# Kernel tuning notes

Measured on AMD Instinct MI355X. Metric: run time of the kernel, lower is better.

Reference implementation:

```python
import jax, jax.numpy as jnp
import numpy as np

D_MODEL = 1024
EXPAND = 2
D_INNER = D_MODEL * EXPAND
KERNEL = 4
EPS = 1e-5


def setup_inputs() -> dict:
    key = jax.random.key(0)
    ks = jax.random.split(key, 8)
    B, L = 2, 4096
    x = jax.random.normal(ks[0], (B, L, D_MODEL), dtype=jnp.float32)
    norm_w = jnp.ones((D_MODEL,), jnp.float32)
    norm_b = jnp.zeros((D_MODEL,), jnp.float32)
    # torch Linear weight layout [out, in]
    in_proj_w = jax.random.normal(ks[1], (2 * D_INNER, D_MODEL), jnp.float32) / np.sqrt(D_MODEL)
    # depthwise Conv1d weight [d_inner, 1, K]
    conv_w = jax.random.normal(ks[2], (D_INNER, 1, KERNEL), jnp.float32) / np.sqrt(KERNEL)
    conv_b = jax.random.normal(ks[3], (D_INNER,), jnp.float32) * 0.02
    gate_w = jax.random.normal(ks[4], (D_INNER, D_INNER), jnp.float32) / np.sqrt(D_INNER)
    gate_b = jnp.zeros((D_INNER,), jnp.float32)
    out_proj_w = jax.random.normal(ks[5], (D_MODEL, D_INNER), jnp.float32) / np.sqrt(D_INNER)
    return {"x": x, "norm_w": norm_w, "norm_b": norm_b, "in_proj_w": in_proj_w,
            "conv_w": conv_w, "conv_b": conv_b, "gate_w": gate_w, "gate_b": gate_b,
            "out_proj_w": out_proj_w}


def _layernorm(x, w, b):
    mu = jnp.mean(x, axis=-1, keepdims=True)
    var = jnp.var(x, axis=-1, keepdims=True)
    return (x - mu) * jax.lax.rsqrt(var + EPS) * w + b


def _glru(x, norm_w, norm_b, in_proj_w, conv_w, conv_b, gate_w, gate_b, out_proj_w):
    B, L, D = x.shape
    residual = x
    xn = _layernorm(x, norm_w, norm_b)
    xz = jnp.einsum('bld,ed->ble', xn, in_proj_w)  # [B,L,2*d_inner]
    x_inner, z = jnp.split(xz, 2, axis=-1)
    # causal depthwise conv: torch pads 3 both sides then slices [:L] == left-pad 3
    lhs = jnp.transpose(x_inner, (0, 2, 1))  # [B, C, L]
    conv = jax.lax.conv_general_dilated(
        lhs, conv_w, window_strides=(1,), padding=[(KERNEL - 1, 0)],
        feature_group_count=D_INNER,
        dimension_numbers=('NCH', 'OIH', 'NCH'))
    x_conv = jnp.transpose(conv, (0, 2, 1)) + conv_b  # [B, L, C]
    x_conv = jax.nn.silu(x_conv)
    a = jax.nn.sigmoid(jnp.einsum('blc,ec->ble', x_conv, gate_w) + gate_b)
    b = (1.0 - a) * x_conv
    # h_t = a_t * h_{t-1} + b_t, h_0 prior = 0 -> parallel associative scan
    def combine(e1, e2):
        a1, b1 = e1
        a2, b2 = e2
        return a1 * a2, a2 * b1 + b2
    _, y = jax.lax.associative_scan(combine, (a, b), axis=1)
    y = y * jax.nn.silu(z)
    return residual + jnp.einsum('blc,dc->bld', y, out_proj_w)


def reference(x, norm_w, norm_b, in_proj_w, conv_w, conv_b, gate_w, gate_b, out_proj_w):
    return _glru(x, norm_w, norm_b, in_proj_w, conv_w, conv_b, gate_w, gate_b, out_proj_w)
```

## Files before the change

### kernel.cpp

```cpp
#include <hip/hip_runtime.h>
#include <cstdint>

#define D_MODEL 1024
#define D_INNER 2048
#define LSEQ    4096
#define BATCH   2
#define M_ROWS  (BATCH * LSEQ)
#define CHUNK   128
#define NCHUNK  (LSEQ / CHUNK)

typedef unsigned short u16;
typedef __bf16 bf16x8 __attribute__((ext_vector_type(8)));
typedef float f32x4 __attribute__((ext_vector_type(4)));
typedef u16 u16x4 __attribute__((ext_vector_type(4)));

__device__ __forceinline__ u16 f2bf(float f) {
  union { float f; unsigned u; } x; x.f = f;
  unsigned u = x.u;
  unsigned r = (u + 0x7FFFu + ((u >> 16) & 1u)) >> 16;
  return (u16)r;
}
__device__ __forceinline__ float bf2f(u16 h) {
  union { unsigned u; float f; } x; x.u = ((unsigned)h) << 16;
  return x.f;
}
__device__ __forceinline__ float sigmoidf_(float v) { return 1.0f / (1.0f + expf(-v)); }
__device__ __forceinline__ float siluf_(float v)    { return v / (1.0f + expf(-v)); }

__device__ __forceinline__ void gl_lds16(const void* g, void* l) {
  __builtin_amdgcn_global_load_lds(
      (const __attribute__((address_space(1))) void*)g,
      (__attribute__((address_space(3))) void*)l, 16, 0, 0);
}

#define SBAR()   asm volatile("s_barrier" ::: "memory")
#define WAITV0() asm volatile("s_waitcnt vmcnt(0)" ::: "memory")
#define WAITL0() do { asm volatile("s_waitcnt lgkmcnt(0)" ::: "memory"); __builtin_amdgcn_sched_barrier(0); } while (0)

__global__ void __launch_bounds__(256)
cast_bf16_kernel(const float* __restrict__ in, u16* __restrict__ out, int n4) {
  int i = blockIdx.x * 256 + threadIdx.x;
  if (i < n4) {
    float4 v = ((const float4*)in)[i];
    u16x4 o;
    o.x = f2bf(v.x); o.y = f2bf(v.y); o.z = f2bf(v.z); o.w = f2bf(v.w);
    ((u16x4*)out)[i] = o;
  }
}

__global__ void __launch_bounds__(256)
ln_kernel(const float* __restrict__ x, const float* __restrict__ w,
          const float* __restrict__ b, u16* __restrict__ xn) {
  const int row = blockIdx.x;
  const int t = threadIdx.x;
  const float4 v = ((const float4*)(x + (size_t)row * D_MODEL))[t];
  float s  = v.x + v.y + v.z + v.w;
  float ss = v.x * v.x + v.y * v.y + v.z * v.z + v.w * v.w;
#pragma unroll
  for (int o = 32; o > 0; o >>= 1) {
    s  += __shfl_xor(s, o);
    ss += __shfl_xor(ss, o);
  }
  __shared__ float red[8];
  const int wid = t >> 6, lane = t & 63;
  if (lane == 0) { red[wid] = s; red[4 + wid] = ss; }
  __syncthreads();
  s  = red[0] + red[1] + red[2] + red[3];
  ss = red[4] + red[5] + red[6] + red[7];
  const float mu  = s * (1.0f / D_MODEL);
  const float var = ss * (1.0f / D_MODEL) - mu * mu;
  const float rs  = rsqrtf(var + 1e-5f);
  const float4 wv = ((const float4*)w)[t];
  const float4 bv = ((const float4*)b)[t];
  u16x4 o4;
  o4.x = f2bf((v.x - mu) * rs * wv.x + bv.x);
  o4.y = f2bf((v.y - mu) * rs * wv.y + bv.y);
  o4.z = f2bf((v.z - mu) * rs * wv.z + bv.z);
  o4.w = f2bf((v.w - mu) * rs * wv.w + bv.w);
  ((u16x4*)(xn + (size_t)row * D_MODEL))[t] = o4;
}

#define MFMA_BF16 __builtin_amdgcn_mfma_f32_16x16x32_bf16

template<int EPI>
__global__ void __launch_bounds__(512, 2)
gemm256(const u16* __restrict__ A, const u16* __restrict__ Bm,
        int M, int N, int K,
        const float* __restrict__ ef, float* __restrict__ of,
        u16* __restrict__ ob0, u16* __restrict__ ob1) {
  __shared__ __align__(1024) char lds[131072];
  const int tid  = threadIdx.x;
  const int wid  = tid >> 6, lane = tid & 63;
  const int nbx  = N >> 8;
  const int nwg  = nbx * (M >> 8);
  const int bid  = blockIdx.x;
  const int cpx  = nwg >> 3;
  const int swz  = (bid & 7) * cpx + (bid >> 3);
  const int bx   = swz % nbx, by = swz / nbx;
  const size_t m0 = (size_t)by << 8, n0 = (size_t)bx << 8;

  const int wr = wid >> 2, wc = wid & 3;
  const size_t rb = (size_t)K * 2;
  const size_t rj = (size_t)64 * rb;

  const int srow  = lane >> 3;
  const int sslot = ((lane & 7) ^ srow) << 4;
  const char* gA = (const char*)A  + (m0 + (size_t)(wid * 8 + srow)) * rb + sslot;
  const char* gB = (const char*)Bm + (n0 + (size_t)(wid * 8 + srow)) * rb + sslot;
  const int sdst = wid * 1024;

  const int q    = lane >> 4;
  const int r15  = lane & 15;
  const int cswz0 = (q * 16)      ^ ((lane & 7) << 4);
  const int cswz1 = (64 + q * 16) ^ ((lane & 7) << 4);
  const int paoff = (wr * 128 + r15) * 128;
  const int pboff = (wc * 64  + r15) * 128;

  f32x4 acc[8][4] = {};
  const int nk = K >> 6;

  {
    const char* a = gA; const char* b = gB;
#pragma unroll
    for (int i = 0; i < 4; ++i) {
      gl_lds16(a, lds + sdst + i * 8192);
      gl_lds16(b, lds + 65536 + sdst + i * 8192);
      a += rj; b += rj;
    }
  }
  WAITV0();
  SBAR();

  int kb = 128;
  for (int t = 0; t < nk; ++t) {
    const int cur = t & 1;
    const char* At = lds + cur * 32768;
    const char* Bt = lds + 65536 + cur * 32768;
    char* An = lds + (cur ^ 1) * 32768;
    char* Bn = lds + 65536 + (cur ^ 1) * 32768;
    const bool pf = (t + 1 < nk);

    bf16x8 af[4][2], b0[2][2], b1[2][2];

    if (pf) {
      gl_lds16(gA + kb,      An + sdst);
      gl_lds16(gA + kb + rj, An + sdst + 8192);
      gl_lds16(gB + kb,      Bn + sdst);
      gl_lds16(gB + kb + rj, Bn + sdst + 8192);
    }
#pragma unroll
    for (int mi = 0; mi < 4; ++mi) {
      af[mi][0] = *(const bf16x8*)(At + paoff + mi * 2048 + cswz0);
      af[mi][1] = *(const bf16x8*)(At + paoff + mi * 2048 + cswz1);
    }
#pragma unroll
    for (int ni = 0; ni < 2; ++ni) {
      b0[ni][0] = *(const bf16x8*)(Bt + pboff + ni * 2048 + cswz0);
      b0[ni][1] = *(const bf16x8*)(Bt + pboff + ni * 2048 + cswz1);
    }
    SBAR();
    WAITL0();
    __builtin_amdgcn_s_setprio(1);
#pragma unroll
    for (int mi = 0; mi < 4; ++mi)
#pragma unroll
      for (int ni = 0; ni < 2; ++ni) {
        acc[mi][ni] = MFMA_BF16(af[mi][0], b0[ni][0], acc[mi][ni], 0, 0, 0);
        acc[mi][ni] = MFMA_BF16(af[mi][1], b0[ni][1], acc[mi][ni], 0, 0, 0);
      }
    __builtin_amdgcn_s_setprio(0);
    SBAR();

    if (pf) {
      gl_lds16(gA + kb + 2 * rj, An + sdst + 16384);
      gl_lds16(gA + kb + 3 * rj, An + sdst + 24576);
      gl_lds16(gB + kb + 2 * rj, Bn + sdst + 16384);
      gl_lds16(gB + kb + 3 * rj, Bn + sdst + 24576);
    }
#pragma unroll
    for (int ni = 0; ni < 2; ++ni) {
      b1[ni][0] = *(const bf16x8*)(Bt + pboff + (ni + 2) * 2048 + cswz0);
      b1[ni][1] = *(const bf16x8*)(Bt + pboff + (ni + 2) * 2048 + cswz1);
    }
    SBAR();
    WAITL0();
    __builtin_amdgcn_s_setprio(1);
#pragma unroll
    for (int mi = 0; mi < 4; ++mi)
#pragma unroll
      for (int ni = 0; ni < 2; ++ni) {
        acc[mi][ni + 2] = MFMA_BF16(af[mi][0], b1[ni][0], acc[mi][ni + 2], 0, 0, 0);
        acc[mi][ni + 2] = MFMA_BF16(af[mi][1], b1[ni][1], acc[mi][ni + 2], 0, 0, 0);
      }
    __builtin_amdgcn_s_setprio(0);
    SBAR();

#pragma unroll
    for (int mi = 0; mi < 4; ++mi) {
      af[mi][0] = *(const bf16x8*)(At + paoff + (mi + 4) * 2048 + cswz0);
      af[mi][1] = *(const bf16x8*)(At + paoff + (mi + 4) * 2048 + cswz1);
    }
    SBAR();
    WAITL0();
    __builtin_amdgcn_s_setprio(1);
#pragma unroll
    for (int mi = 0; mi < 4; ++mi)
#pragma unroll
      for (int ni = 0; ni < 2; ++ni) {
        acc[mi + 4][ni] = MFMA_BF16(af[mi][0], b0[ni][0], acc[mi + 4][ni], 0, 0, 0);
        acc[mi + 4][ni] = MFMA_BF16(af[mi][1], b0[ni][1], acc[mi + 4][ni], 0, 0, 0);
      }
    __builtin_amdgcn_s_setprio(0);
    SBAR();

    __builtin_amdgcn_s_setprio(1);
#pragma unroll
    for (int mi = 0; mi < 4; ++mi)
#pragma unroll
      for (int ni = 0; ni < 2; ++ni) {
        acc[mi + 4][ni + 2] = MFMA_BF16(af[mi][0], b1[ni][0], acc[mi + 4][ni + 2], 0, 0, 0);
        acc[mi + 4][ni + 2] = MFMA_BF16(af[mi][1], b1[ni][1], acc[mi + 4][ni + 2], 0, 0, 0);
      }
    __builtin_amdgcn_s_setprio(0);
    if (pf) WAITV0();
    SBAR();
    kb += 128;
  }

  const int c0 = lane & 15;
  const int r0 = (lane >> 4) << 2;
#pragma unroll
  for (int mi = 0; mi < 8; ++mi) {
#pragma unroll
    for (int ni = 0; ni < 4; ++ni) {
#pragma unroll
      for (int rg = 0; rg < 4; ++rg) {
        const size_t row = m0 + (size_t)(wr * 128 + mi * 16 + r0 + rg);
        const size_t col = n0 + (size_t)(wc * 64 + ni * 16 + c0);
        const float v = acc[mi][ni][rg];
        if (EPI == 0) {
          if (col < (size_t)D_INNER) ob0[row * D_INNER + col] = f2bf(v);
          else                       ob1[row * D_INNER + (col - D_INNER)] = f2bf(siluf_(v));
        } else if (EPI == 1) {
          of[row * (size_t)N + col] = sigmoidf_(v + ef[col]);
        } else {
          of[row * (size_t)N + col] = v + ef[row * (size_t)N + col];
        }
      }
    }
  }
}

__global__ void __launch_bounds__(256)
conv_silu_kernel(const u16* __restrict__ xin, const float* __restrict__ cw,
                 const float* __restrict__ cb, u16* __restrict__ xc) {
  const int c   = blockIdx.x * 256 + threadIdx.x;
  const int l0  = blockIdx.y * 8;
  const int bat = blockIdx.z;
  const size_t base = ((size_t)bat * LSEQ) * D_INNER + c;
  const float w0 = cw[c * 4 + 0], w1 = cw[c * 4 + 1], w2 = cw[c * 4 + 2], w3 = cw[c * 4 + 3];
  const float bb = cb[c];
  float v[11];
#pragma unroll
  for (int i = 0; i < 11; ++i) {
    const int l = l0 - 3 + i;
    v[i] = (l >= 0) ? bf2f(xin[base + (size_t)l * D_INNER]) : 0.0f;
  }
#pragma unroll
  for (int r = 0; r < 8; ++r) {
    const float acc = bb + w0 * v[r] + w1 * v[r + 1] + w2 * v[r + 2] + w3 * v[r + 3];
    xc[base + (size_t)(l0 + r) * D_INNER] = f2bf(siluf_(acc));
  }
}

__global__ void __launch_bounds__(256)
scan_a_kernel(const float* __restrict__ a, const u16* __restrict__ xc,
              float* __restrict__ cA, float* __restrict__ cB) {
  const int c   = blockIdx.x * 256 + threadIdx.x;
  const int ch  = blockIdx.y;
  const int bat = blockIdx.z;
  size_t idx = ((size_t)bat * LSEQ + (size_t)ch * CHUNK) * D_INNER + c;
  float pA = 1.0f, hB = 0.0f;
  for (int t = 0; t < CHUNK; ++t) {
    const float av = a[idx];
    const float bv = (1.0f - av) * bf2f(xc[idx]);
    pA *= av;
    hB = av * hB + bv;
    idx += D_INNER;
  }
  const size_t o = ((size_t)bat * NCHUNK + ch) * D_INNER + c;
  cA[o] = pA; cB[o] = hB;
}

__global__ void __launch_bounds__(256)
scan_b_kernel(const float* __restrict__ cA, const float* __restrict__ cB,
              float* __restrict__ carry) {
  const int tid = blockIdx.x * 256 + threadIdx.x;
  const int bat = tid >> 11;
  const int c   = tid & (D_INNER - 1);
  float h = 0.0f;
  const size_t base = (size_t)bat * NCHUNK * D_INNER + c;
  for (int i = 0; i < NCHUNK; ++i) {
    const size_t o = base + (size_t)i * D_INNER;
    carry[o] = h;
    h = cA[o] * h + cB[o];
  }
}

__global__ void __launch_bounds__(256)
scan_c_kernel(const float* __restrict__ a, const u16* __restrict__ xc,
              const u16* __restrict__ sz, const float* __restrict__ carry,
              u16* __restrict__ yg) {
  const int c   = blockIdx.x * 256 + threadIdx.x;
  const int ch  = blockIdx.y;
  const int bat = blockIdx.z;
  float h = carry[((size_t)bat * NCHUNK + ch) * D_INNER + c];
  size_t idx = ((size_t)bat * LSEQ + (size_t)ch * CHUNK) * D_INNER + c;
  for (int t = 0; t < CHUNK; ++t) {
    const float av = a[idx];
    const float bv = (1.0f - av) * bf2f(xc[idx]);
    h = av * h + bv;
    yg[idx] = f2bf(h * bf2f(sz[idx]));
    idx += D_INNER;
  }
}

extern "C" void kernel_launch(void* const* d_in, const int* in_sizes, int n_in,
                              void* d_out, int out_size, void* d_ws, size_t ws_size,
                              hipStream_t stream) {
  const float* x         = (const float*)d_in[0];
  const float* norm_w    = (const float*)d_in[1];
  const float* norm_b    = (const float*)d_in[2];
  const float* in_proj_w = (const float*)d_in[3];
  const float* conv_w    = (const float*)d_in[4];
  const float* conv_b    = (const float*)d_in[5];
  const float* gate_w    = (const float*)d_in[6];
  const float* gate_b    = (const float*)d_in[7];
  const float* out_proj_w= (const float*)d_in[8];
  float* out = (float*)d_out;

  char* p = (char*)d_ws;
  u16* xn      = (u16*)p; p += (size_t)M_ROWS * D_MODEL * 2;
  u16* w_in    = (u16*)p; p += (size_t)2 * D_INNER * D_MODEL * 2;
  u16* w_gate  = (u16*)p; p += (size_t)D_INNER * D_INNER * 2;
  u16* w_out   = (u16*)p; p += (size_t)D_MODEL * D_INNER * 2;
  u16* x_inner = (u16*)p; p += (size_t)M_ROWS * D_INNER * 2;
  u16* szb     = (u16*)p; p += (size_t)M_ROWS * D_INNER * 2;
  u16* xconv   = (u16*)p; p += (size_t)M_ROWS * D_INNER * 2;
  float* a_f   = (float*)p; p += (size_t)M_ROWS * D_INNER * 4;
  u16* yg      = (u16*)p; p += (size_t)M_ROWS * D_INNER * 2;
  float* cA    = (float*)p; p += (size_t)BATCH * NCHUNK * D_INNER * 4;
  float* cB    = (float*)p; p += (size_t)BATCH * NCHUNK * D_INNER * 4;
  float* carry = (float*)p; p += (size_t)BATCH * NCHUNK * D_INNER * 4;
  if ((size_t)(p - (char*)d_ws) > ws_size) return;

  cast_bf16_kernel<<<dim3(2 * D_INNER * D_MODEL / 4 / 256), 256, 0, stream>>>(in_proj_w, w_in, 2 * D_INNER * D_MODEL / 4);
  cast_bf16_kernel<<<dim3(D_INNER * D_INNER / 4 / 256), 256, 0, stream>>>(gate_w, w_gate, D_INNER * D_INNER / 4);
  cast_bf16_kernel<<<dim3(D_MODEL * D_INNER / 4 / 256), 256, 0, stream>>>(out_proj_w, w_out, D_MODEL * D_INNER / 4);

  ln_kernel<<<dim3(M_ROWS), 256, 0, stream>>>(x, norm_w, norm_b, xn);

  gemm256<0><<<dim3((M_ROWS / 256) * (2 * D_INNER / 256)), 512, 0, stream>>>(
      xn, w_in, M_ROWS, 2 * D_INNER, D_MODEL, nullptr, nullptr, x_inner, szb);

  conv_silu_kernel<<<dim3(D_INNER / 256, LSEQ / 8, BATCH), 256, 0, stream>>>(x_inner, conv_w, conv_b, xconv);

  gemm256<1><<<dim3((M_ROWS / 256) * (D_INNER / 256)), 512, 0, stream>>>(
      xconv, w_gate, M_ROWS, D_INNER, D_INNER, gate_b, a_f, nullptr, nullptr);

  scan_a_kernel<<<dim3(D_INNER / 256, NCHUNK, BATCH), 256, 0, stream>>>(a_f, xconv, cA, cB);
  scan_b_kernel<<<dim3(BATCH * D_INNER / 256), 256, 0, stream>>>(cA, cB, carry);
  scan_c_kernel<<<dim3(D_INNER / 256, NCHUNK, BATCH), 256, 0, stream>>>(a_f, xconv, szb, carry, yg);

  gemm256<2><<<dim3((M_ROWS / 256) * (D_MODEL / 256)), 512, 0, stream>>>(
      yg, w_out, M_ROWS, D_MODEL, D_INNER, x, out, nullptr, nullptr);
}
```

Measured before the change: 342.6 us.

## Store gate pre-activation as bf16, fuse sigmoid into scans, issue all prefetches earlier

```diff
diff --git a/kernel.cpp b/kernel.cpp
--- a/kernel.cpp
+++ b/kernel.cpp
@@ -35,6 +35,8 @@
 
 #define SBAR()   asm volatile("s_barrier" ::: "memory")
 #define WAITV0() asm volatile("s_waitcnt vmcnt(0)" ::: "memory")
+#define WAITV2() asm volatile("s_waitcnt vmcnt(2)" ::: "memory")
+#define WAITV8() asm volatile("s_waitcnt vmcnt(8)" ::: "memory")
 #define WAITL0() do { asm volatile("s_waitcnt lgkmcnt(0)" ::: "memory"); __builtin_amdgcn_sched_barrier(0); } while (0)
 
 __global__ void __launch_bounds__(256)
@@ -131,7 +133,7 @@
   WAITV0();
   SBAR();
 
-  int kb = 128;
+  size_t kb = 128;
   for (int t = 0; t < nk; ++t) {
     const int cur = t & 1;
     const char* At = lds + cur * 32768;
@@ -143,10 +145,14 @@
     bf16x8 af[4][2], b0[2][2], b1[2][2];
 
     if (pf) {
-      gl_lds16(gA + kb,      An + sdst);
-      gl_lds16(gA + kb + rj, An + sdst + 8192);
-      gl_lds16(gB + kb,      Bn + sdst);
-      gl_lds16(gB + kb + rj, Bn + sdst + 8192);
+      gl_lds16(gA + kb,          An + sdst);
+      gl_lds16(gA + kb + 2 * rj, An + sdst + 16384);
+      gl_lds16(gB + kb,          Bn + sdst);
+      gl_lds16(gB + kb + rj,     Bn + sdst + 8192);
+      gl_lds16(gB + kb + 2 * rj, Bn + sdst + 16384);
+      gl_lds16(gB + kb + 3 * rj, Bn + sdst + 24576);
+      gl_lds16(gA + kb + rj,     An + sdst + 8192);
+      gl_lds16(gA + kb + 3 * rj, An + sdst + 24576);
     }
 #pragma unroll
     for (int mi = 0; mi < 4; ++mi) {
@@ -171,12 +177,6 @@
     __builtin_amdgcn_s_setprio(0);
     SBAR();
 
-    if (pf) {
-      gl_lds16(gA + kb + 2 * rj, An + sdst + 16384);
-      gl_lds16(gA + kb + 3 * rj, An + sdst + 24576);
-      gl_lds16(gB + kb + 2 * rj, Bn + sdst + 16384);
-      gl_lds16(gB + kb + 3 * rj, Bn + sdst + 24576);
-    }
 #pragma unroll
     for (int ni = 0; ni < 2; ++ni) {
       b1[ni][0] = *(const bf16x8*)(Bt + pboff + (ni + 2) * 2048 + cswz0);
@@ -193,6 +193,7 @@
         acc[mi][ni + 2] = MFMA_BF16(af[mi][1], b1[ni][1], acc[mi][ni + 2], 0, 0, 0);
       }
     __builtin_amdgcn_s_setprio(0);
+    if (pf) { WAITV8(); } else { WAITV0(); }
     SBAR();
 
 #pragma unroll
@@ -222,7 +223,7 @@
         acc[mi + 4][ni + 2] = MFMA_BF16(af[mi][1], b1[ni][1], acc[mi + 4][ni + 2], 0, 0, 0);
       }
     __builtin_amdgcn_s_setprio(0);
-    if (pf) WAITV0();
+    if (pf) { WAITV2(); }
     SBAR();
     kb += 128;
   }
@@ -242,7 +243,7 @@
           if (col < (size_t)D_INNER) ob0[row * D_INNER + col] = f2bf(v);
           else                       ob1[row * D_INNER + (col - D_INNER)] = f2bf(siluf_(v));
         } else if (EPI == 1) {
-          of[row * (size_t)N + col] = sigmoidf_(v + ef[col]);
+          ob0[row * (size_t)N + col] = f2bf(v);
         } else {
           of[row * (size_t)N + col] = v + ef[row * (size_t)N + col];
         }
@@ -274,22 +275,27 @@
 }
 
 __global__ void __launch_bounds__(256)
-scan_a_kernel(const float* __restrict__ a, const u16* __restrict__ xc,
+scan_a_kernel(const u16* __restrict__ g, const u16* __restrict__ xc,
+              const float* __restrict__ gbias,
               float* __restrict__ cA, float* __restrict__ cB) {
-  const int c   = blockIdx.x * 256 + threadIdx.x;
+  const int c   = (blockIdx.x * 256 + threadIdx.x) * 2;
   const int ch  = blockIdx.y;
   const int bat = blockIdx.z;
+  const float bb0 = gbias[c], bb1 = gbias[c + 1];
   size_t idx = ((size_t)bat * LSEQ + (size_t)ch * CHUNK) * D_INNER + c;
-  float pA = 1.0f, hB = 0.0f;
+  float pA0 = 1.0f, hB0 = 0.0f, pA1 = 1.0f, hB1 = 0.0f;
   for (int t = 0; t < CHUNK; ++t) {
-    const float av = a[idx];
-    const float bv = (1.0f - av) * bf2f(xc[idx]);
-    pA *= av;
-    hB = av * hB + bv;
+    const ushort2 gg = *(const ushort2*)(g + idx);
+    const ushort2 xx = *(const ushort2*)(xc + idx);
+    const float a0 = sigmoidf_(bf2f(gg.x) + bb0);
+    const float a1 = sigmoidf_(bf2f(gg.y) + bb1);
+    pA0 *= a0; hB0 = a0 * hB0 + (1.0f - a0) * bf2f(xx.x);
+    pA1 *= a1; hB1 = a1 * hB1 + (1.0f - a1) * bf2f(xx.y);
     idx += D_INNER;
   }
   const size_t o = ((size_t)bat * NCHUNK + ch) * D_INNER + c;
-  cA[o] = pA; cB[o] = hB;
+  *(float2*)(cA + o) = make_float2(pA0, pA1);
+  *(float2*)(cB + o) = make_float2(hB0, hB1);
 }
 
 __global__ void __launch_bounds__(256)
@@ -308,19 +314,28 @@
 }
 
 __global__ void __launch_bounds__(256)
-scan_c_kernel(const float* __restrict__ a, const u16* __restrict__ xc,
-              const u16* __restrict__ sz, const float* __restrict__ carry,
-              u16* __restrict__ yg) {
-  const int c   = blockIdx.x * 256 + threadIdx.x;
+scan_c_kernel(const u16* __restrict__ g, const u16* __restrict__ xc,
+              const u16* __restrict__ sz, const float* __restrict__ gbias,
+              const float* __restrict__ carry, u16* __restrict__ yg) {
+  const int c   = (blockIdx.x * 256 + threadIdx.x) * 2;
   const int ch  = blockIdx.y;
   const int bat = blockIdx.z;
-  float h = carry[((size_t)bat * NCHUNK + ch) * D_INNER + c];
+  const float bb0 = gbias[c], bb1 = gbias[c + 1];
+  const float2 h2 = *(const float2*)(carry + ((size_t)bat * NCHUNK + ch) * D_INNER + c);
+  float h0 = h2.x, h1 = h2.y;
   size_t idx = ((size_t)bat * LSEQ + (size_t)ch * CHUNK) * D_INNER + c;
   for (int t = 0; t < CHUNK; ++t) {
-    const float av = a[idx];
-    const float bv = (1.0f - av) * bf2f(xc[idx]);
-    h = av * h + bv;
-    yg[idx] = f2bf(h * bf2f(sz[idx]));
+    const ushort2 gg = *(const ushort2*)(g + idx);
+    const ushort2 xx = *(const ushort2*)(xc + idx);
+    const ushort2 zz = *(const ushort2*)(sz + idx);
+    const float a0 = sigmoidf_(bf2f(gg.x) + bb0);
+    const float a1 = sigmoidf_(bf2f(gg.y) + bb1);
+    h0 = a0 * h0 + (1.0f - a0) * bf2f(xx.x);
+    h1 = a1 * h1 + (1.0f - a1) * bf2f(xx.y);
+    ushort2 o2;
+    o2.x = f2bf(h0 * bf2f(zz.x));
+    o2.y = f2bf(h1 * bf2f(zz.y));
+    *(ushort2*)(yg + idx) = o2;
     idx += D_INNER;
   }
 }
@@ -347,7 +362,7 @@
   u16* x_inner = (u16*)p; p += (size_t)M_ROWS * D_INNER * 2;
   u16* szb     = (u16*)p; p += (size_t)M_ROWS * D_INNER * 2;
   u16* xconv   = (u16*)p; p += (size_t)M_ROWS * D_INNER * 2;
-  float* a_f   = (float*)p; p += (size_t)M_ROWS * D_INNER * 4;
+  u16* gbuf    = (u16*)p; p += (size_t)M_ROWS * D_INNER * 2;
   u16* yg      = (u16*)p; p += (size_t)M_ROWS * D_INNER * 2;
   float* cA    = (float*)p; p += (size_t)BATCH * NCHUNK * D_INNER * 4;
   float* cB    = (float*)p; p += (size_t)BATCH * NCHUNK * D_INNER * 4;
@@ -366,11 +381,11 @@
   conv_silu_kernel<<<dim3(D_INNER / 256, LSEQ / 8, BATCH), 256, 0, stream>>>(x_inner, conv_w, conv_b, xconv);
 
   gemm256<1><<<dim3((M_ROWS / 256) * (D_INNER / 256)), 512, 0, stream>>>(
-      xconv, w_gate, M_ROWS, D_INNER, D_INNER, gate_b, a_f, nullptr, nullptr);
-
-  scan_a_kernel<<<dim3(D_INNER / 256, NCHUNK, BATCH), 256, 0, stream>>>(a_f, xconv, cA, cB);
+      xconv, w_gate, M_ROWS, D_INNER, D_INNER, nullptr, nullptr, gbuf, nullptr);
+
+  scan_a_kernel<<<dim3(D_INNER / 512, NCHUNK, BATCH), 256, 0, stream>>>(gbuf, xconv, gate_b, cA, cB);
   scan_b_kernel<<<dim3(BATCH * D_INNER / 256), 256, 0, stream>>>(cA, cB, carry);
-  scan_c_kernel<<<dim3(D_INNER / 256, NCHUNK, BATCH), 256, 0, stream>>>(a_f, xconv, szb, carry, yg);
+  scan_c_kernel<<<dim3(D_INNER / 512, NCHUNK, BATCH), 256, 0, stream>>>(gbuf, xconv, szb, gate_b, carry, yg);
 
   gemm256<2><<<dim3((M_ROWS / 256) * (D_MODEL / 256)), 512, 0, stream>>>(
       yg, w_out, M_ROWS, D_MODEL, D_INNER, x, out, nullptr, nullptr);
```

Result: slower. 368.0 us (+7.4%).
